# Performance work log

Measured on AMD Instinct MI355X. Metric: run time of the kernel, lower is better.

## Reference

```python
import jax, jax.numpy as jnp
import numpy as np


def setup_inputs() -> dict:
    key = jax.random.key(0)
    k1, k2, k3, k4, k5 = jax.random.split(key, 5)
    return {
        "d1": jax.random.normal(k1, (2, 4096, 512), dtype=jnp.float32),
        "d2": jax.random.normal(k2, (2, 512, 4096), dtype=jnp.float32),
        "d3": jax.random.normal(k3, (2, 4096, 512), dtype=jnp.float32),
        "d4": jax.random.normal(k4, (512, 512), dtype=jnp.float32),
        "d5": jax.random.normal(k5, (1, 512), dtype=jnp.float32),
    }


def reference(d1, d2, d3, d4, d5):
    # attention core: scores = d1 @ d2 -> [2, 4096, 4096]
    scores = jnp.einsum('bsd,bdt->bst', d1, d2)
    attn = jax.nn.softmax(scores, axis=2)
    # weighted values: [2, 4096, 512]
    ctx = jnp.einsum('bst,btd->bsd', attn, d3)
    # flatten batch*seq and apply final projection with bias (addmm)
    x = ctx.reshape(8192, 512)
    return d5 + x @ d4  # d5 [1,512] broadcasts over rows
```

## Files before the change

kernel.cpp:

```cpp
#include <hip/hip_runtime.h>

typedef unsigned short u16;
typedef __attribute__((ext_vector_type(8))) short short8;
typedef __attribute__((ext_vector_type(4))) float f32x4;

#define MFMA16(a, b, c) __builtin_amdgcn_mfma_f32_16x16x32_bf16((a), (b), (c), 0, 0, 0)

constexpr int Bb = 2, Ss = 4096, Tt = 4096, Dd = 512;
constexpr int BM = 64, BN = 64, TP = 4;
constexpr int TPART = Tt / TP;
constexpr int TCH = TPART / BN;

constexpr size_t SZ_BF = (size_t)Bb * Ss * Dd * 2;
constexpr size_t O_QH  = 0;
constexpr size_t O_QL  = O_QH + SZ_BF;
constexpr size_t O_D2TH = O_QL + SZ_BF;
constexpr size_t O_D2TL = O_D2TH + SZ_BF;
constexpr size_t O_D3T  = O_D2TL + SZ_BF;
constexpr size_t O_D4T  = O_D3T + SZ_BF;
constexpr size_t O_CTX  = O_D4T + (size_t)512 * 512 * 2;
constexpr size_t O_OP   = O_CTX + SZ_BF;
constexpr size_t O_MP   = O_OP + (size_t)TP * SZ_BF;
constexpr size_t O_LP   = O_MP + (size_t)TP * Bb * Ss * 4;

__device__ __forceinline__ u16 f2bf(float x) {
  union { float f; unsigned u; } v; v.f = x;
  unsigned r = v.u + 0x7fffu + ((v.u >> 16) & 1u);
  return (u16)(r >> 16);
}
__device__ __forceinline__ float bf2f(u16 h) {
  union { unsigned u; float f; } v; v.u = ((unsigned)h) << 16;
  return v.f;
}

__global__ void cvt_split_kernel(const float* __restrict__ in,
                                 u16* __restrict__ outh, u16* __restrict__ outl) {
  const int i = blockIdx.x * 256 + threadIdx.x;
  float4 v = ((const float4*)in)[i];
  ushort4 hh, ll;
  hh.x = f2bf(v.x); ll.x = f2bf(v.x - bf2f(hh.x));
  hh.y = f2bf(v.y); ll.y = f2bf(v.y - bf2f(hh.y));
  hh.z = f2bf(v.z); ll.z = f2bf(v.z - bf2f(hh.z));
  hh.w = f2bf(v.w); ll.w = f2bf(v.w - bf2f(hh.w));
  ((ushort4*)outh)[i] = hh;
  ((ushort4*)outl)[i] = ll;
}

__global__ void transpose_split_kernel(const float* __restrict__ in,
                                       u16* __restrict__ outh,
                                       u16* __restrict__ outl,
                                       int R, int C) {
  __shared__ float tile[32][33];
  int b = blockIdx.z;
  const float* inb = in + (size_t)b * R * C;
  int x = blockIdx.x * 32 + threadIdx.x;
  int y0 = blockIdx.y * 32;
  for (int j = threadIdx.y; j < 32; j += 8)
    tile[j][threadIdx.x] = inb[(size_t)(y0 + j) * C + x];
  __syncthreads();
  size_t ob = (size_t)b * C * R;
  for (int j = threadIdx.y; j < 32; j += 8) {
    float v = tile[threadIdx.x][j];
    size_t oi = ob + (size_t)(blockIdx.x * 32 + j) * R + (y0 + threadIdx.x);
    u16 h = f2bf(v);
    outh[oi] = h;
    if (outl) outl[oi] = f2bf(v - bf2f(h));
  }
}

__global__ __launch_bounds__(256, 2)
void flash_part_kernel(const u16* __restrict__ qh_g,
                       const u16* __restrict__ ql_g,
                       const u16* __restrict__ d2th,
                       const u16* __restrict__ d2tl,
                       const u16* __restrict__ d3t,
                       u16* __restrict__ opart,
                       float* __restrict__ mpart,
                       float* __restrict__ lpart) {
  __shared__ u16 kh[64 * 136], kl[64 * 136];
  __shared__ u16 vb[128 * 72];
  __shared__ u16 ph[64 * 72];

  const int tid = threadIdx.x;
  const int wave = tid >> 6, lane = tid & 63, quad = lane >> 4, l15 = lane & 15;
  const int m0 = wave * 16;
  const int s0 = blockIdx.x * BM, tp = blockIdx.y, b = blockIdx.z;

  f32x4 o_acc[32];
#pragma unroll
  for (int i = 0; i < 32; i++) o_acc[i] = (f32x4){0.f, 0.f, 0.f, 0.f};
  float m_r[4] = {-INFINITY, -INFINITY, -INFINITY, -INFINITY};
  float l_r[4] = {0.f, 0.f, 0.f, 0.f};

  const u16* qh_row = qh_g + ((size_t)b * Ss + s0 + m0 + l15) * Dd + quad * 8;
  const u16* ql_row = ql_g + ((size_t)b * Ss + s0 + m0 + l15) * Dd + quad * 8;
  const u16* kh_b = d2th + (size_t)b * Tt * Dd;
  const u16* kl_b = d2tl + (size_t)b * Tt * Dd;
  const u16* v_b  = d3t  + (size_t)b * Dd * Tt;

  const int krow = tid >> 2, kcol = (tid & 3) * 32;
  const int vrow = tid >> 1, vcol = (tid & 1) * 32;

  for (int tc = 0; tc < TCH; tc++) {
    const int t0 = tp * TPART + tc * BN;
    f32x4 s_acc[4];
#pragma unroll
    for (int nt = 0; nt < 4; nt++) s_acc[nt] = (f32x4){0.f, 0.f, 0.f, 0.f};

    for (int ds = 0; ds < 4; ds++) {
      const int d0 = ds * 128;
      __syncthreads();
      {
        const u16* sh = kh_b + (size_t)(t0 + krow) * Dd + d0 + kcol;
        const u16* sl = kl_b + (size_t)(t0 + krow) * Dd + d0 + kcol;
        u16* dh = &kh[krow * 136 + kcol];
        u16* dl = &kl[krow * 136 + kcol];
#pragma unroll
        for (int u = 0; u < 32; u += 8) {
          *(uint4*)(dh + u) = *(const uint4*)(sh + u);
          *(uint4*)(dl + u) = *(const uint4*)(sl + u);
        }
      }
      __syncthreads();
      short8 ah[4], al[4];
#pragma unroll
      for (int ks = 0; ks < 4; ks++) {
        ah[ks] = *(const short8*)(qh_row + d0 + ks * 32);
        al[ks] = *(const short8*)(ql_row + d0 + ks * 32);
      }
#pragma unroll
      for (int ks = 0; ks < 4; ks++) {
        const int kk = ks * 32 + quad * 8;
#pragma unroll
        for (int nt = 0; nt < 4; nt++) {
          short8 bh = *(const short8*)&kh[(nt * 16 + l15) * 136 + kk];
          short8 bl = *(const short8*)&kl[(nt * 16 + l15) * 136 + kk];
          s_acc[nt] = MFMA16(ah[ks], bh, s_acc[nt]);
          s_acc[nt] = MFMA16(al[ks], bh, s_acc[nt]);
          s_acc[nt] = MFMA16(ah[ks], bl, s_acc[nt]);
        }
      }
    }

    float alpha[4], psum[4];
#pragma unroll
    for (int r = 0; r < 4; r++) {
      float v = fmaxf(fmaxf(s_acc[0][r], s_acc[1][r]), fmaxf(s_acc[2][r], s_acc[3][r]));
      v = fmaxf(v, __shfl_xor(v, 1));
      v = fmaxf(v, __shfl_xor(v, 2));
      v = fmaxf(v, __shfl_xor(v, 4));
      v = fmaxf(v, __shfl_xor(v, 8));
      float mn = fmaxf(m_r[r], v);
      alpha[r] = __expf(m_r[r] - mn);
      m_r[r] = mn;
      psum[r] = 0.f;
    }
#pragma unroll
    for (int nt = 0; nt < 4; nt++) {
#pragma unroll
      for (int r = 0; r < 4; r++) {
        float p = __expf(s_acc[nt][r] - m_r[r]);
        psum[r] += p;
        ph[(m0 + quad * 4 + r) * 72 + nt * 16 + l15] = f2bf(p);
      }
    }
#pragma unroll
    for (int r = 0; r < 4; r++) {
      float v = psum[r];
      v += __shfl_xor(v, 1);
      v += __shfl_xor(v, 2);
      v += __shfl_xor(v, 4);
      v += __shfl_xor(v, 8);
      l_r[r] = l_r[r] * alpha[r] + v;
    }
#pragma unroll
    for (int j = 0; j < 32; j++) {
#pragma unroll
      for (int r = 0; r < 4; r++) o_acc[j][r] *= alpha[r];
    }

#pragma unroll
    for (int nc = 0; nc < 4; nc++) {
      __syncthreads();
      {
        const u16* sv = v_b + (size_t)(nc * 128 + vrow) * Tt + t0 + vcol;
        u16* dv = &vb[vrow * 72 + vcol];
#pragma unroll
        for (int u = 0; u < 32; u += 8) *(uint4*)(dv + u) = *(const uint4*)(sv + u);
      }
      __syncthreads();
#pragma unroll
      for (int ks = 0; ks < 2; ks++) {
        const int kk = ks * 32 + quad * 8;
        short8 ap = *(const short8*)&ph[(m0 + l15) * 72 + kk];
#pragma unroll
        for (int nt = 0; nt < 8; nt++) {
          short8 bv = *(const short8*)&vb[(nt * 16 + l15) * 72 + kk];
          o_acc[nc * 8 + nt] = MFMA16(ap, bv, o_acc[nc * 8 + nt]);
        }
      }
    }
  }

  const size_t obase = (((size_t)tp * Bb + b) * Ss + s0) * Dd;
#pragma unroll
  for (int j = 0; j < 32; j++) {
    const int col = (j >> 3) * 128 + (j & 7) * 16 + l15;
#pragma unroll
    for (int r = 0; r < 4; r++) {
      const int row = m0 + quad * 4 + r;
      opart[obase + (size_t)row * Dd + col] = f2bf(o_acc[j][r]);
    }
  }
  if (l15 == 0) {
    const size_t sbase = ((size_t)tp * Bb + b) * Ss + s0;
#pragma unroll
    for (int r = 0; r < 4; r++) {
      const int row = m0 + quad * 4 + r;
      mpart[sbase + row] = m_r[r];
      lpart[sbase + row] = l_r[r];
    }
  }
}

__global__ void combine_kernel(const u16* __restrict__ opart,
                               const float* __restrict__ mpart,
                               const float* __restrict__ lpart,
                               u16* __restrict__ ctx) {
  const int idx = blockIdx.x * blockDim.x + threadIdx.x;
  const int vpr = Dd / 8;
  const int row = idx / vpr;
  const int dv = (idx % vpr) * 8;
  float mv[TP], mM = -INFINITY;
#pragma unroll
  for (int p = 0; p < TP; p++) {
    mv[p] = mpart[(size_t)p * Bb * Ss + row];
    mM = fmaxf(mM, mv[p]);
  }
  float w[TP], denom = 0.f;
#pragma unroll
  for (int p = 0; p < TP; p++) {
    float e = __expf(mv[p] - mM);
    w[p] = e;
    denom += e * lpart[(size_t)p * Bb * Ss + row];
  }
  const float inv = 1.0f / denom;
  float acc[8];
#pragma unroll
  for (int e = 0; e < 8; e++) acc[e] = 0.f;
#pragma unroll
  for (int p = 0; p < TP; p++) {
    uint4 raw = *(const uint4*)&opart[(size_t)p * Bb * Ss * Dd + (size_t)row * Dd + dv];
    const u16* u = (const u16*)&raw;
#pragma unroll
    for (int e = 0; e < 8; e++) acc[e] += w[p] * bf2f(u[e]);
  }
  u16 outv[8];
#pragma unroll
  for (int e = 0; e < 8; e++) outv[e] = f2bf(acc[e] * inv);
  *(uint4*)&ctx[(size_t)row * Dd + dv] = *(const uint4*)outv;
}

__global__ __launch_bounds__(256, 2)
void proj_kernel(const u16* __restrict__ ctx,
                 const u16* __restrict__ d4t,
                 const float* __restrict__ d5,
                 float* __restrict__ out) {
  __shared__ u16 a_lds[128 * 40], b_lds[128 * 40];
  const int tid = threadIdx.x;
  const int wave = tid >> 6, lane = tid & 63, quad = lane >> 4, l15 = lane & 15;
  const int m0w = (wave & 1) * 64, n0w = (wave >> 1) * 64;
  const int bm = blockIdx.x, bn = blockIdx.y;
  f32x4 acc[4][4];
#pragma unroll
  for (int i = 0; i < 4; i++)
#pragma unroll
    for (int j = 0; j < 4; j++) acc[i][j] = (f32x4){0.f, 0.f, 0.f, 0.f};

  const int srow = tid >> 2, scol = (tid & 3) * 8;
  for (int kt = 0; kt < 16; kt++) {
    const int k0 = kt * 32;
    __syncthreads();
#pragma unroll
    for (int pass = 0; pass < 2; pass++) {
      const int row = srow + pass * 64;
      *(uint4*)&a_lds[row * 40 + scol] =
          *(const uint4*)&ctx[(size_t)(bm * 128 + row) * Dd + k0 + scol];
      *(uint4*)&b_lds[row * 40 + scol] =
          *(const uint4*)&d4t[(size_t)(bn * 128 + row) * Dd + k0 + scol];
    }
    __syncthreads();
    short8 af[4], bfr[4];
#pragma unroll
    for (int i = 0; i < 4; i++)
      af[i] = *(const short8*)&a_lds[(m0w + 16 * i + l15) * 40 + quad * 8];
#pragma unroll
    for (int j = 0; j < 4; j++)
      bfr[j] = *(const short8*)&b_lds[(n0w + 16 * j + l15) * 40 + quad * 8];
#pragma unroll
    for (int i = 0; i < 4; i++)
#pragma unroll
      for (int j = 0; j < 4; j++) acc[i][j] = MFMA16(af[i], bfr[j], acc[i][j]);
  }
#pragma unroll
  for (int j = 0; j < 4; j++) {
    const int colg = bn * 128 + n0w + 16 * j + l15;
    const float bias = d5[colg];
#pragma unroll
    for (int i = 0; i < 4; i++) {
#pragma unroll
      for (int r = 0; r < 4; r++) {
        const int rowg = bm * 128 + m0w + 16 * i + quad * 4 + r;
        out[(size_t)rowg * 512 + colg] = acc[i][j][r] + bias;
      }
    }
  }
}

extern "C" void kernel_launch(void* const* d_in, const int* in_sizes, int n_in,
                              void* d_out, int out_size, void* d_ws, size_t ws_size,
                              hipStream_t stream) {
  (void)in_sizes; (void)n_in; (void)out_size; (void)ws_size;
  const float* d1 = (const float*)d_in[0];
  const float* d2 = (const float*)d_in[1];
  const float* d3 = (const float*)d_in[2];
  const float* d4 = (const float*)d_in[3];
  const float* d5 = (const float*)d_in[4];
  float* out = (float*)d_out;
  char* ws = (char*)d_ws;

  u16* qh_g = (u16*)(ws + O_QH);
  u16* ql_g = (u16*)(ws + O_QL);
  u16* d2th = (u16*)(ws + O_D2TH);
  u16* d2tl = (u16*)(ws + O_D2TL);
  u16* d3t  = (u16*)(ws + O_D3T);
  u16* d4t  = (u16*)(ws + O_D4T);
  u16* ctx  = (u16*)(ws + O_CTX);
  u16* opart = (u16*)(ws + O_OP);
  float* mpart = (float*)(ws + O_MP);
  float* lpart = (float*)(ws + O_LP);

  cvt_split_kernel<<<(Bb * Ss * Dd / 4) / 256, 256, 0, stream>>>(d1, qh_g, ql_g);
  transpose_split_kernel<<<dim3(128, 16, 2), dim3(32, 8), 0, stream>>>(d2, d2th, d2tl, 512, 4096);
  transpose_split_kernel<<<dim3(16, 128, 2), dim3(32, 8), 0, stream>>>(d3, d3t, nullptr, 4096, 512);
  transpose_split_kernel<<<dim3(16, 16, 1), dim3(32, 8), 0, stream>>>(d4, d4t, nullptr, 512, 512);

  flash_part_kernel<<<dim3(Ss / BM, TP, Bb), 256, 0, stream>>>(qh_g, ql_g, d2th, d2tl, d3t,
                                                               opart, mpart, lpart);
  combine_kernel<<<(Bb * Ss * Dd / 8) / 256, 256, 0, stream>>>(opart, mpart, lpart, ctx);
  proj_kernel<<<dim3(64, 4), 256, 0, stream>>>(ctx, d4t, d5, out);
}
```

Before: 516.4 us.

## Double-buffer K/V tiles in flash kernel with register prefetch, fuse prep kernels

Flattens the flash attention loop into a single sequence of stages (four K sub-chunks, then four V sub-chunks per T chunk). The next stage's tile is prefetched into registers while the current one is computed, then written into a second LDS buffer, so each stage needs one barrier instead of two. The o_acc rescale is skipped when every alpha in the wave equals 1. The four conversion and transpose kernels are merged into one launch that dispatches on block index. The cost is extra register pressure from the 8-entry uint4 prefetch array and more shared memory from the double buffers, which could lower occupancy at launch_bounds(256,2).

```diff
diff --git a/kernel.cpp b/kernel.cpp
--- a/kernel.cpp
+++ b/kernel.cpp
@@ -10,10 +10,11 @@
 constexpr int BM = 64, BN = 64, TP = 4;
 constexpr int TPART = Tt / TP;
 constexpr int TCH = TPART / BN;
+constexpr int NSTAGE = TCH * 8;
 
 constexpr size_t SZ_BF = (size_t)Bb * Ss * Dd * 2;
-constexpr size_t O_QH  = 0;
-constexpr size_t O_QL  = O_QH + SZ_BF;
+constexpr size_t O_QH   = 0;
+constexpr size_t O_QL   = O_QH + SZ_BF;
 constexpr size_t O_D2TH = O_QL + SZ_BF;
 constexpr size_t O_D2TL = O_D2TH + SZ_BF;
 constexpr size_t O_D3T  = O_D2TL + SZ_BF;
@@ -33,38 +34,55 @@
   return v.f;
 }
 
-__global__ void cvt_split_kernel(const float* __restrict__ in,
-                                 u16* __restrict__ outh, u16* __restrict__ outl) {
-  const int i = blockIdx.x * 256 + threadIdx.x;
-  float4 v = ((const float4*)in)[i];
-  ushort4 hh, ll;
-  hh.x = f2bf(v.x); ll.x = f2bf(v.x - bf2f(hh.x));
-  hh.y = f2bf(v.y); ll.y = f2bf(v.y - bf2f(hh.y));
-  hh.z = f2bf(v.z); ll.z = f2bf(v.z - bf2f(hh.z));
-  hh.w = f2bf(v.w); ll.w = f2bf(v.w - bf2f(hh.w));
-  ((ushort4*)outh)[i] = hh;
-  ((ushort4*)outl)[i] = ll;
-}
-
-__global__ void transpose_split_kernel(const float* __restrict__ in,
-                                       u16* __restrict__ outh,
-                                       u16* __restrict__ outl,
-                                       int R, int C) {
-  __shared__ float tile[32][33];
-  int b = blockIdx.z;
-  const float* inb = in + (size_t)b * R * C;
-  int x = blockIdx.x * 32 + threadIdx.x;
-  int y0 = blockIdx.y * 32;
-  for (int j = threadIdx.y; j < 32; j += 8)
-    tile[j][threadIdx.x] = inb[(size_t)(y0 + j) * C + x];
+__device__ __forceinline__ void transpose_sp(const float* __restrict__ in,
+                                             u16* __restrict__ outh,
+                                             u16* __restrict__ outl, int R, int C,
+                                             int bx, int by, int bz,
+                                             int tx, int ty, float* tile) {
+  const float* inb = in + (size_t)bz * R * C;
+  const int x = bx * 32 + tx;
+  const int y0 = by * 32;
+  for (int j = ty; j < 32; j += 8)
+    tile[j * 33 + tx] = inb[(size_t)(y0 + j) * C + x];
   __syncthreads();
-  size_t ob = (size_t)b * C * R;
-  for (int j = threadIdx.y; j < 32; j += 8) {
-    float v = tile[threadIdx.x][j];
-    size_t oi = ob + (size_t)(blockIdx.x * 32 + j) * R + (y0 + threadIdx.x);
+  const size_t ob = (size_t)bz * C * R;
+  for (int j = ty; j < 32; j += 8) {
+    float v = tile[tx * 33 + j];
+    size_t oi = ob + (size_t)(bx * 32 + j) * R + (y0 + tx);
     u16 h = f2bf(v);
     outh[oi] = h;
     if (outl) outl[oi] = f2bf(v - bf2f(h));
+  }
+}
+
+__global__ void prep_kernel(const float* __restrict__ d1, const float* __restrict__ d2,
+                            const float* __restrict__ d3, const float* __restrict__ d4,
+                            u16* __restrict__ qh, u16* __restrict__ ql,
+                            u16* __restrict__ d2th, u16* __restrict__ d2tl,
+                            u16* __restrict__ d3t, u16* __restrict__ d4t) {
+  __shared__ float tile[32 * 33];
+  const int bid = blockIdx.x;
+  const int tid = threadIdx.x;
+  const int tx = tid & 31, ty = tid >> 5;
+  if (bid < 4096) {
+    const int i = bid * 256 + tid;
+    float4 v = ((const float4*)d1)[i];
+    ushort4 hh, ll;
+    hh.x = f2bf(v.x); ll.x = f2bf(v.x - bf2f(hh.x));
+    hh.y = f2bf(v.y); ll.y = f2bf(v.y - bf2f(hh.y));
+    hh.z = f2bf(v.z); ll.z = f2bf(v.z - bf2f(hh.z));
+    hh.w = f2bf(v.w); ll.w = f2bf(v.w - bf2f(hh.w));
+    ((ushort4*)qh)[i] = hh;
+    ((ushort4*)ql)[i] = ll;
+  } else if (bid < 8192) {
+    const int t = bid - 4096;
+    transpose_sp(d2, d2th, d2tl, 512, 4096, t & 127, (t >> 7) & 15, t >> 11, tx, ty, tile);
+  } else if (bid < 12288) {
+    const int t = bid - 8192;
+    transpose_sp(d3, d3t, nullptr, 4096, 512, t & 15, (t >> 4) & 127, t >> 11, tx, ty, tile);
+  } else {
+    const int t = bid - 12288;
+    transpose_sp(d4, d4t, nullptr, 512, 512, t & 15, t >> 4, 0, tx, ty, tile);
   }
 }
 
@@ -77,8 +95,7 @@
                        u16* __restrict__ opart,
                        float* __restrict__ mpart,
                        float* __restrict__ lpart) {
-  __shared__ u16 kh[64 * 136], kl[64 * 136];
-  __shared__ u16 vb[128 * 72];
+  __shared__ u16 bufs[2][17408];
   __shared__ u16 ph[64 * 72];
 
   const int tid = threadIdx.x;
@@ -89,6 +106,7 @@
   f32x4 o_acc[32];
 #pragma unroll
   for (int i = 0; i < 32; i++) o_acc[i] = (f32x4){0.f, 0.f, 0.f, 0.f};
+  f32x4 s_acc[4];
   float m_r[4] = {-INFINITY, -INFINITY, -INFINITY, -INFINITY};
   float l_r[4] = {0.f, 0.f, 0.f, 0.f};
 
@@ -101,27 +119,52 @@
   const int krow = tid >> 2, kcol = (tid & 3) * 32;
   const int vrow = tid >> 1, vcol = (tid & 1) * 32;
 
-  for (int tc = 0; tc < TCH; tc++) {
-    const int t0 = tp * TPART + tc * BN;
-    f32x4 s_acc[4];
-#pragma unroll
-    for (int nt = 0; nt < 4; nt++) s_acc[nt] = (f32x4){0.f, 0.f, 0.f, 0.f};
-
-    for (int ds = 0; ds < 4; ds++) {
-      const int d0 = ds * 128;
-      __syncthreads();
-      {
-        const u16* sh = kh_b + (size_t)(t0 + krow) * Dd + d0 + kcol;
-        const u16* sl = kl_b + (size_t)(t0 + krow) * Dd + d0 + kcol;
-        u16* dh = &kh[krow * 136 + kcol];
-        u16* dl = &kl[krow * 136 + kcol];
-#pragma unroll
-        for (int u = 0; u < 32; u += 8) {
-          *(uint4*)(dh + u) = *(const uint4*)(sh + u);
-          *(uint4*)(dl + u) = *(const uint4*)(sl + u);
-        }
-      }
-      __syncthreads();
+  {
+    const int t0 = tp * TPART;
+    const u16* sh = kh_b + (size_t)(t0 + krow) * Dd + kcol;
+    const u16* sl = kl_b + (size_t)(t0 + krow) * Dd + kcol;
+    u16* dh = &bufs[0][krow * 136 + kcol];
+#pragma unroll
+    for (int u = 0; u < 32; u += 8) {
+      *(uint4*)(dh + u) = *(const uint4*)(sh + u);
+      *(uint4*)(dh + 8704 + u) = *(const uint4*)(sl + u);
+    }
+  }
+  __syncthreads();
+
+  int cur = 0;
+  for (int s = 0; s < NSTAGE; s++) {
+    const int sub = s & 7;
+    const bool has_next = (s + 1 < NSTAGE);
+    const int nsub = (s + 1) & 7;
+    const bool next_is_k = (nsub < 4);
+
+    uint4 pf[8];
+    if (has_next) {
+      const int ntc = (s + 1) >> 3;
+      const int nt0 = tp * TPART + ntc * BN;
+      if (next_is_k) {
+        const u16* sh = kh_b + (size_t)(nt0 + krow) * Dd + nsub * 128 + kcol;
+        const u16* sl = kl_b + (size_t)(nt0 + krow) * Dd + nsub * 128 + kcol;
+#pragma unroll
+        for (int u = 0; u < 4; u++) {
+          pf[u] = *(const uint4*)(sh + u * 8);
+          pf[4 + u] = *(const uint4*)(sl + u * 8);
+        }
+      } else {
+        const u16* sv = v_b + (size_t)((nsub - 4) * 128 + vrow) * Tt + nt0 + vcol;
+#pragma unroll
+        for (int u = 0; u < 4; u++) pf[u] = *(const uint4*)(sv + u * 8);
+      }
+    }
+
+    const u16* bb = bufs[cur];
+    if (sub < 4) {
+      if (sub == 0) {
+#pragma unroll
+        for (int nt = 0; nt < 4; nt++) s_acc[nt] = (f32x4){0.f, 0.f, 0.f, 0.f};
+      }
+      const int d0 = sub * 128;
       short8 ah[4], al[4];
 #pragma unroll
       for (int ks = 0; ks < 4; ks++) {
@@ -133,73 +176,83 @@
         const int kk = ks * 32 + quad * 8;
 #pragma unroll
         for (int nt = 0; nt < 4; nt++) {
-          short8 bh = *(const short8*)&kh[(nt * 16 + l15) * 136 + kk];
-          short8 bl = *(const short8*)&kl[(nt * 16 + l15) * 136 + kk];
+          short8 bh = *(const short8*)&bb[(nt * 16 + l15) * 136 + kk];
+          short8 bl = *(const short8*)&bb[8704 + (nt * 16 + l15) * 136 + kk];
           s_acc[nt] = MFMA16(ah[ks], bh, s_acc[nt]);
           s_acc[nt] = MFMA16(al[ks], bh, s_acc[nt]);
           s_acc[nt] = MFMA16(ah[ks], bl, s_acc[nt]);
         }
       }
-    }
-
-    float alpha[4], psum[4];
-#pragma unroll
-    for (int r = 0; r < 4; r++) {
-      float v = fmaxf(fmaxf(s_acc[0][r], s_acc[1][r]), fmaxf(s_acc[2][r], s_acc[3][r]));
-      v = fmaxf(v, __shfl_xor(v, 1));
-      v = fmaxf(v, __shfl_xor(v, 2));
-      v = fmaxf(v, __shfl_xor(v, 4));
-      v = fmaxf(v, __shfl_xor(v, 8));
-      float mn = fmaxf(m_r[r], v);
-      alpha[r] = __expf(m_r[r] - mn);
-      m_r[r] = mn;
-      psum[r] = 0.f;
-    }
-#pragma unroll
-    for (int nt = 0; nt < 4; nt++) {
-#pragma unroll
-      for (int r = 0; r < 4; r++) {
-        float p = __expf(s_acc[nt][r] - m_r[r]);
-        psum[r] += p;
-        ph[(m0 + quad * 4 + r) * 72 + nt * 16 + l15] = f2bf(p);
-      }
-    }
-#pragma unroll
-    for (int r = 0; r < 4; r++) {
-      float v = psum[r];
-      v += __shfl_xor(v, 1);
-      v += __shfl_xor(v, 2);
-      v += __shfl_xor(v, 4);
-      v += __shfl_xor(v, 8);
-      l_r[r] = l_r[r] * alpha[r] + v;
-    }
-#pragma unroll
-    for (int j = 0; j < 32; j++) {
-#pragma unroll
-      for (int r = 0; r < 4; r++) o_acc[j][r] *= alpha[r];
-    }
-
-#pragma unroll
-    for (int nc = 0; nc < 4; nc++) {
-      __syncthreads();
-      {
-        const u16* sv = v_b + (size_t)(nc * 128 + vrow) * Tt + t0 + vcol;
-        u16* dv = &vb[vrow * 72 + vcol];
-#pragma unroll
-        for (int u = 0; u < 32; u += 8) *(uint4*)(dv + u) = *(const uint4*)(sv + u);
-      }
-      __syncthreads();
+      if (sub == 3) {
+        float alpha[4], psum[4];
+#pragma unroll
+        for (int r = 0; r < 4; r++) {
+          float v = fmaxf(fmaxf(s_acc[0][r], s_acc[1][r]), fmaxf(s_acc[2][r], s_acc[3][r]));
+          v = fmaxf(v, __shfl_xor(v, 1));
+          v = fmaxf(v, __shfl_xor(v, 2));
+          v = fmaxf(v, __shfl_xor(v, 4));
+          v = fmaxf(v, __shfl_xor(v, 8));
+          float mn = fmaxf(m_r[r], v);
+          alpha[r] = __expf(m_r[r] - mn);
+          m_r[r] = mn;
+          psum[r] = 0.f;
+        }
+#pragma unroll
+        for (int nt = 0; nt < 4; nt++) {
+#pragma unroll
+          for (int r = 0; r < 4; r++) {
+            float p = __expf(s_acc[nt][r] - m_r[r]);
+            psum[r] += p;
+            ph[(m0 + quad * 4 + r) * 72 + nt * 16 + l15] = f2bf(p);
+          }
+        }
+#pragma unroll
+        for (int r = 0; r < 4; r++) {
+          float v = psum[r];
+          v += __shfl_xor(v, 1);
+          v += __shfl_xor(v, 2);
+          v += __shfl_xor(v, 4);
+          v += __shfl_xor(v, 8);
+          l_r[r] = l_r[r] * alpha[r] + v;
+        }
+        bool need = (alpha[0] != 1.f) | (alpha[1] != 1.f) | (alpha[2] != 1.f) | (alpha[3] != 1.f);
+        if (__any(need)) {
+#pragma unroll
+          for (int j = 0; j < 32; j++)
+#pragma unroll
+            for (int r = 0; r < 4; r++) o_acc[j][r] *= alpha[r];
+        }
+      }
+    } else {
+      const int nc = sub - 4;
 #pragma unroll
       for (int ks = 0; ks < 2; ks++) {
         const int kk = ks * 32 + quad * 8;
         short8 ap = *(const short8*)&ph[(m0 + l15) * 72 + kk];
 #pragma unroll
         for (int nt = 0; nt < 8; nt++) {
-          short8 bv = *(const short8*)&vb[(nt * 16 + l15) * 72 + kk];
+          short8 bv = *(const short8*)&bb[(nt * 16 + l15) * 72 + kk];
           o_acc[nc * 8 + nt] = MFMA16(ap, bv, o_acc[nc * 8 + nt]);
         }
       }
     }
+
+    if (has_next) {
+      if (next_is_k) {
+        u16* dh = &bufs[cur ^ 1][krow * 136 + kcol];
+#pragma unroll
+        for (int u = 0; u < 4; u++) {
+          *(uint4*)(dh + u * 8) = pf[u];
+          *(uint4*)(dh + 8704 + u * 8) = pf[4 + u];
+        }
+      } else {
+        u16* dv = &bufs[cur ^ 1][vrow * 72 + vcol];
+#pragma unroll
+        for (int u = 0; u < 4; u++) *(uint4*)(dv + u * 8) = pf[u];
+      }
+    }
+    __syncthreads();
+    cur ^= 1;
   }
 
   const size_t obase = (((size_t)tp * Bb + b) * Ss + s0) * Dd;
@@ -340,11 +393,7 @@
   float* mpart = (float*)(ws + O_MP);
   float* lpart = (float*)(ws + O_LP);
 
-  cvt_split_kernel<<<(Bb * Ss * Dd / 4) / 256, 256, 0, stream>>>(d1, qh_g, ql_g);
-  transpose_split_kernel<<<dim3(128, 16, 2), dim3(32, 8), 0, stream>>>(d2, d2th, d2tl, 512, 4096);
-  transpose_split_kernel<<<dim3(16, 128, 2), dim3(32, 8), 0, stream>>>(d3, d3t, nullptr, 4096, 512);
-  transpose_split_kernel<<<dim3(16, 16, 1), dim3(32, 8), 0, stream>>>(d4, d4t, nullptr, 512, 512);
-
+  prep_kernel<<<12544, 256, 0, stream>>>(d1, d2, d3, d4, qh_g, ql_g, d2th, d2tl, d3t, d4t);
   flash_part_kernel<<<dim3(Ss / BM, TP, Bb), 256, 0, stream>>>(qh_g, ql_g, d2th, d2tl, d3t,
                                                                opart, mpart, lpart);
   combine_kernel<<<(Bb * Ss * Dd / 8) / 256, 256, 0, stream>>>(opart, mpart, lpart, ctx);
```

Measured after the change: 1.181 ms. 129% more time.
